# Performance work log

Measured on AMD Instinct MI355X. Metric: run time of the kernel, lower is better.

## Reference

```python
import jax, jax.numpy as jnp
import numpy as np

B, S, HID = 2, 2048, 1024
H, D = 16, 64  # head_dim = HID // H
MAXPOS = 2048


def setup_inputs() -> dict:
    key = jax.random.key(0)
    ks = jax.random.split(key, 9)
    s = 0.02
    return {
        "hidden_states": jax.random.normal(ks[0], (B, S, HID), jnp.float32),
        "attention_mask": jnp.zeros((B, 1, 1, S), jnp.float32),
        "Wq": jax.random.normal(ks[1], (HID, HID), jnp.float32) * s,
        "bq": jnp.zeros((HID,), jnp.float32),
        "Wk": jax.random.normal(ks[2], (HID, HID), jnp.float32) * s,
        "bk": jnp.zeros((HID,), jnp.float32),
        "Wv": jax.random.normal(ks[3], (HID, HID), jnp.float32) * s,
        "bv": jnp.zeros((HID,), jnp.float32),
        "dist_emb": jax.random.normal(ks[4], (2 * MAXPOS - 1, D), jnp.float32) * s,
    }


def reference(hidden_states, attention_mask, Wq, bq, Wk, bk, Wv, bv, dist_emb):
    b, s, _ = hidden_states.shape

    def heads(x):  # [B,S,HID] -> [B,H,S,D]
        return x.reshape(b, s, H, D).transpose(0, 2, 1, 3)

    q = heads(hidden_states @ Wq.T + bq)
    k = heads(hidden_states @ Wk.T + bk)
    v = heads(hidden_states @ Wv.T + bv)

    # raw scores [B,H,L,R]
    scores = jnp.einsum("bhld,bhrd->bhlr", q, k)

    # relative_key_query position bias
    pos_l = jnp.arange(s)[:, None]
    pos_r = jnp.arange(s)[None, :]
    distance = pos_l - pos_r + (MAXPOS - 1)  # [L,R]
    pos_emb = dist_emb[distance]  # [L,R,D]
    rel_q = jnp.einsum("bhld,lrd->bhlr", q, pos_emb)
    rel_k = jnp.einsum("bhrd,lrd->bhlr", k, pos_emb)
    scores = scores + rel_q + rel_k

    scores = scores / jnp.sqrt(jnp.asarray(D, scores.dtype))
    scores = scores + attention_mask  # additive mask broadcast [B,1,1,R]

    probs = jax.nn.softmax(scores, axis=-1)  # dropout p=0 -> identity
    ctx = jnp.einsum("bhlr,bhrd->bhld", probs, v)  # [B,H,L,D]
    ctx = ctx.transpose(0, 2, 1, 3).reshape(b, s, H * D)
    return ctx
```

## Files before the change

kernel.cpp:

```cpp
#include <hip/hip_runtime.h>

typedef __bf16 bf16_t;
typedef __bf16 bf16x8 __attribute__((ext_vector_type(8)));
typedef __bf16 bf16x4v __attribute__((ext_vector_type(4)));
typedef float floatx4 __attribute__((ext_vector_type(4)));

#define MFMA16(a, b, c) __builtin_amdgcn_mfma_f32_16x16x32_bf16((a), (b), (c), 0, 0, 0)

constexpr int S_ = 2048;
constexpr int HID_ = 1024;
constexpr int HH = 16;
constexpr int DD = 64;
constexpr float ALPHA = 0.125f * 1.44269504f;
constexpr float LOG2E = 1.44269504f;

__device__ __forceinline__ void async_copy16(const bf16_t* g, bf16_t* l) {
  __builtin_amdgcn_global_load_lds((const __attribute__((address_space(1))) unsigned int*)g,
                                   (__attribute__((address_space(3))) unsigned int*)l, 16, 0, 0);
}

__global__ __launch_bounds__(256) void cvt_all_kernel(
    const float* __restrict__ h, const float* __restrict__ wq, const float* __restrict__ wk,
    const float* __restrict__ wv, const float* __restrict__ de, bf16_t* __restrict__ hb,
    bf16_t* __restrict__ wb, bf16_t* __restrict__ eb) {
  int v = blockIdx.x * 256 + threadIdx.x;
  if (v >= 1900528) return;
  const float* src;
  bf16_t* dst;
  int off;
  if (v < 1048576) {
    src = h; dst = hb; off = v;
  } else if (v < 1310720) {
    src = wq; dst = wb; off = v - 1048576;
  } else if (v < 1572864) {
    src = wk; dst = wb + 1048576; off = v - 1310720;
  } else if (v < 1835008) {
    src = wv; dst = wb + 2097152; off = v - 1572864;
  } else {
    src = de; dst = eb; off = v - 1835008;
  }
  float4 f = *(const float4*)(src + (size_t)off * 4);
  bf16x4v p = {(bf16_t)f.x, (bf16_t)f.y, (bf16_t)f.z, (bf16_t)f.w};
  *(bf16x4v*)(dst + (size_t)off * 4) = p;
}

__global__ __launch_bounds__(256) void cvt_e_kernel(const float* __restrict__ src,
                                                    bf16_t* __restrict__ dst, int n) {
  int i = blockIdx.x * 256 + threadIdx.x;
  if (i < n) dst[i] = (bf16_t)src[i];
}

__global__ __launch_bounds__(256) void qkv_gemm3_kernel(
    const bf16_t* __restrict__ hb, const bf16_t* __restrict__ wb,
    const float* __restrict__ bq, const float* __restrict__ bk, const float* __restrict__ bv,
    bf16_t* __restrict__ qb, bf16_t* __restrict__ kb, bf16_t* __restrict__ vb) {
  __shared__ alignas(16) bf16_t As[128 * 64];
  __shared__ alignas(16) bf16_t Bs[128 * 64];
  const int tid = threadIdx.x;
  const int lane = tid & 63, wid = tid >> 6;
  const int l15 = lane & 15, quad = lane >> 4;
  const int m0 = blockIdx.x * 128, n0 = blockIdx.y * 128;
  const int wm = (wid >> 1) * 64, wn = (wid & 1) * 64;
  floatx4 acc[4][4] = {};
  const int srow = wid * 8 + (lane >> 3);
  const int scol = (lane & 7) * 8;
  const bf16_t* aptr = hb + (size_t)(m0 + srow) * HID_ + scol;
  const bf16_t* bptr = wb + (size_t)(n0 + srow) * HID_ + scol;
  bf16_t* As_w = As + (size_t)(wid * 8) * 64;
  bf16_t* Bs_w = Bs + (size_t)(wid * 8) * 64;

  for (int k0 = 0; k0 < HID_; k0 += 64) {
    __syncthreads();
#pragma unroll
    for (int p = 0; p < 4; ++p) {
      async_copy16(aptr + k0 + (size_t)p * 32 * HID_, As_w + p * 32 * 64);
      async_copy16(bptr + k0 + (size_t)p * 32 * HID_, Bs_w + p * 32 * 64);
    }
    __syncthreads();
    bf16x8 af[4][2], bfv[4][2];
#pragma unroll
    for (int t = 0; t < 4; ++t)
#pragma unroll
      for (int kh = 0; kh < 2; ++kh) {
        af[t][kh] = *(const bf16x8*)&As[(wm + t * 16 + l15) * 64 + kh * 32 + quad * 8];
        bfv[t][kh] = *(const bf16x8*)&Bs[(wn + t * 16 + l15) * 64 + kh * 32 + quad * 8];
      }
#pragma unroll
    for (int mt = 0; mt < 4; ++mt)
#pragma unroll
      for (int nt = 0; nt < 4; ++nt) {
        acc[mt][nt] = MFMA16(af[mt][0], bfv[nt][0], acc[mt][nt]);
        acc[mt][nt] = MFMA16(af[mt][1], bfv[nt][1], acc[mt][nt]);
      }
  }

  const int z = n0 >> 10;
  const float* bias = (z == 0) ? bq : (z == 1) ? bk : bv;
  bf16_t* out = (z == 0) ? qb : (z == 1) ? kb : vb;
  const float scl = (z == 0) ? ALPHA : 1.0f;
#pragma unroll
  for (int nt = 0; nt < 4; ++nt) {
    int oo = (n0 & 1023) + wn + nt * 16 + l15;
    float bvs = bias[oo];
    int h = oo >> 6, d = oo & 63;
#pragma unroll
    for (int mt = 0; mt < 4; ++mt) {
      int sb = m0 + wm + mt * 16 + quad * 4;
      int b = sb >> 11, s = sb & 2047;
      if (z != 2) {
        bf16_t* dst = out + (((size_t)(b * HH + h) * S_ + s) * DD + d);
#pragma unroll
        for (int i = 0; i < 4; ++i) dst[(size_t)i * DD] = (bf16_t)((acc[mt][nt][i] + bvs) * scl);
      } else {
        bf16_t* dst = out + (((size_t)(b * HH + h) * DD + d) * S_ + s);
        bf16x4v pk = {(bf16_t)(acc[mt][nt][0] + bvs), (bf16_t)(acc[mt][nt][1] + bvs),
                      (bf16_t)(acc[mt][nt][2] + bvs), (bf16_t)(acc[mt][nt][3] + bvs)};
        *(bf16x4v*)dst = pk;
      }
    }
  }
}

__global__ __launch_bounds__(256) void qkv_gemm_kernel(
    const float* __restrict__ X, const float* __restrict__ W,
    const float* __restrict__ bias, bf16_t* __restrict__ out, int transposed, float scl) {
  __shared__ alignas(16) bf16_t As[128][40];
  __shared__ alignas(16) bf16_t Bs[128][40];
  const int tid = threadIdx.x;
  const int lane = tid & 63, wid = tid >> 6;
  const int l15 = lane & 15, quad = lane >> 4;
  const int m0 = blockIdx.x * 128, n0 = blockIdx.y * 128;
  const int wm = (wid >> 1) * 64, wn = (wid & 1) * 64;
  floatx4 acc[4][4] = {};
  const int srow = tid >> 1, scol = (tid & 1) * 16;
  const float* aptr = X + (size_t)(m0 + srow) * HID_ + scol;
  const float* bptr = W + (size_t)(n0 + srow) * HID_ + scol;

  for (int k0 = 0; k0 < HID_; k0 += 32) {
    __syncthreads();
    {
      const float4* a4 = (const float4*)(aptr + k0);
      float4 f0 = a4[0], f1 = a4[1], f2 = a4[2], f3 = a4[3];
      bf16x4v p0 = {(bf16_t)f0.x, (bf16_t)f0.y, (bf16_t)f0.z, (bf16_t)f0.w};
      bf16x4v p1 = {(bf16_t)f1.x, (bf16_t)f1.y, (bf16_t)f1.z, (bf16_t)f1.w};
      bf16x4v p2 = {(bf16_t)f2.x, (bf16_t)f2.y, (bf16_t)f2.z, (bf16_t)f2.w};
      bf16x4v p3 = {(bf16_t)f3.x, (bf16_t)f3.y, (bf16_t)f3.z, (bf16_t)f3.w};
      *(bf16x4v*)&As[srow][scol + 0] = p0;
      *(bf16x4v*)&As[srow][scol + 4] = p1;
      *(bf16x4v*)&As[srow][scol + 8] = p2;
      *(bf16x4v*)&As[srow][scol + 12] = p3;
      const float4* b4 = (const float4*)(bptr + k0);
      float4 g0 = b4[0], g1 = b4[1], g2 = b4[2], g3 = b4[3];
      bf16x4v q0 = {(bf16_t)g0.x, (bf16_t)g0.y, (bf16_t)g0.z, (bf16_t)g0.w};
      bf16x4v q1 = {(bf16_t)g1.x, (bf16_t)g1.y, (bf16_t)g1.z, (bf16_t)g1.w};
      bf16x4v q2 = {(bf16_t)g2.x, (bf16_t)g2.y, (bf16_t)g2.z, (bf16_t)g2.w};
      bf16x4v q3 = {(bf16_t)g3.x, (bf16_t)g3.y, (bf16_t)g3.z, (bf16_t)g3.w};
      *(bf16x4v*)&Bs[srow][scol + 0] = q0;
      *(bf16x4v*)&Bs[srow][scol + 4] = q1;
      *(bf16x4v*)&Bs[srow][scol + 8] = q2;
      *(bf16x4v*)&Bs[srow][scol + 12] = q3;
    }
    __syncthreads();
    bf16x8 af[4], bfv[4];
#pragma unroll
    for (int t = 0; t < 4; ++t) af[t] = *(const bf16x8*)&As[wm + t * 16 + l15][quad * 8];
#pragma unroll
    for (int t = 0; t < 4; ++t) bfv[t] = *(const bf16x8*)&Bs[wn + t * 16 + l15][quad * 8];
#pragma unroll
    for (int mt = 0; mt < 4; ++mt)
#pragma unroll
      for (int nt = 0; nt < 4; ++nt)
        acc[mt][nt] = MFMA16(af[mt], bfv[nt], acc[mt][nt]);
  }

#pragma unroll
  for (int nt = 0; nt < 4; ++nt) {
    int o = n0 + wn + nt * 16 + l15;
    float bv = bias[o];
    int h = o >> 6, d = o & 63;
#pragma unroll
    for (int mt = 0; mt < 4; ++mt) {
      int sb = m0 + wm + mt * 16 + quad * 4;
      int b = sb >> 11, s = sb & 2047;
      if (!transposed) {
        bf16_t* dst = out + (((size_t)(b * HH + h) * S_ + s) * DD + d);
#pragma unroll
        for (int i = 0; i < 4; ++i) dst[(size_t)i * DD] = (bf16_t)((acc[mt][nt][i] + bv) * scl);
      } else {
        bf16_t* dst = out + (((size_t)(b * HH + h) * DD + d) * S_ + s);
        bf16x4v pk = {(bf16_t)(acc[mt][nt][0] + bv), (bf16_t)(acc[mt][nt][1] + bv),
                      (bf16_t)(acc[mt][nt][2] + bv), (bf16_t)(acc[mt][nt][3] + bv)};
        *(bf16x4v*)dst = pk;
      }
    }
  }
}

__global__ __launch_bounds__(256, 3) void attn8_kernel(
    const bf16_t* __restrict__ Q, const bf16_t* __restrict__ K,
    const bf16_t* __restrict__ Vt, const bf16_t* __restrict__ E,
    const float* __restrict__ mask, float* __restrict__ out) {
  __shared__ alignas(16) bf16_t Er[128 * 64];
  __shared__ alignas(16) bf16_t Vs[64 * 64];
  __shared__ alignas(16) bf16_t PX[65 * 64];
  __shared__ alignas(16) bf16_t X1t[64][134];
  __shared__ float lsumS[4][64];

  const int tid = threadIdx.x;
  const int lane = tid & 63, wid = tid >> 6;
  const int l15 = lane & 15, quad = lane >> 4;
  const int bh = blockIdx.x & 31, lblk = blockIdx.x >> 5;
  const int l0 = lblk * 64;
  const bf16_t* Qb = Q + (size_t)bh * S_ * DD;
  const bf16_t* Kb = K + (size_t)bh * S_ * DD;
  const bf16_t* Vb = Vt + (size_t)bh * DD * S_;
  const float* maskb = mask + (size_t)(bh >> 4) * S_;

  bf16x8 qB[4][2];
#pragma unroll
  for (int ct = 0; ct < 4; ++ct) {
    const bf16_t* qp = Qb + (size_t)(l0 + ct * 16 + l15) * DD + quad * 8;
    qB[ct][0] = *(const bf16x8*)qp;
    qB[ct][1] = *(const bf16x8*)(qp + 32);
  }

  {
    int rr = tid >> 2, c0 = (tid & 3) * 2;
    int grow = l0 + 2048 + rr;
    if (grow > 4094) grow = 4094;
    const bf16_t* ep = E + (size_t)grow * DD + c0 * 8;
    bf16x8 e0 = *(const bf16x8*)ep;
    bf16x8 e1 = *(const bf16x8*)(ep + 8);
    int slot = (l0 + 2048 + rr) & 127, sw = rr & 7;
    *(bf16x8*)&Er[slot * 64 + (((c0 + 0) ^ sw) << 3)] = e0;
    *(bf16x8*)&Er[slot * 64 + (((c0 + 1) ^ sw) << 3)] = e1;
  }
  __syncthreads();

#pragma unroll
  for (int wt = 0; wt < 4; ++wt) {
    int sr = (l0 + 2048 + wt * 16 + l15) & 127;
    int sw = l15 & 7;
    bf16x8 e0 = *(const bf16x8*)&Er[sr * 64 + ((quad ^ sw) << 3)];
    bf16x8 e1 = *(const bf16x8*)&Er[sr * 64 + (((4 + quad) ^ sw) << 3)];
    floatx4 t1 = {};
    t1 = MFMA16(qB[wid][0], e0, t1);
    t1 = MFMA16(qB[wid][1], e1, t1);
    const int wl = wt * 16 + l15;
#pragma unroll
    for (int i = 0; i < 4; ++i) {
      int ll = wid * 16 + quad * 4 + i;
      int r = ll - wl - 1;
      int col = (r >= 0) ? r : (128 + i);
      X1t[ll][col] = (bf16_t)t1[i];
    }
  }

  floatx4 Oacc[4] = {};
  float lsum[4] = {0.f, 0.f, 0.f, 0.f};

  for (int r0 = 0; r0 < S_; r0 += 64) {
    const int A = l0 - r0 + 1984;
    {
      int rr = tid >> 2, c0 = (tid & 3) * 2;
      const bf16_t* ep = E + (size_t)(A + rr) * DD + c0 * 8;
      bf16x8 e0 = *(const bf16x8*)ep;
      bf16x8 e1 = *(const bf16x8*)(ep + 8);
      int slot = (A + rr) & 127, sw = rr & 7;
      *(bf16x8*)&Er[slot * 64 + (((c0 + 0) ^ sw) << 3)] = e0;
      *(bf16x8*)&Er[slot * 64 + (((c0 + 1) ^ sw) << 3)] = e1;
    }
    const bf16_t* kp = Kb + (size_t)(r0 + wid * 16 + l15) * DD + quad * 8;
    bf16x8 kf0 = *(const bf16x8*)kp;
    bf16x8 kf1 = *(const bf16x8*)(kp + 32);
    float4 m4 = *(const float4*)(maskb + r0 + wid * 16 + quad * 4);
    float mlg[4] = {m4.x * LOG2E, m4.y * LOG2E, m4.z * LOG2E, m4.w * LOG2E};
    __syncthreads();

#pragma unroll
    for (int wt = 0; wt < 8; ++wt) {
      const bool needT1 = (wt < 4);
      const bool needT2 = (wt + wid >= 3) && (wt + wid <= 7);
      if (!(needT1 || needT2)) continue;
      int sr = (A + wt * 16 + l15) & 127;
      int sw = l15 & 7;
      bf16x8 e0 = *(const bf16x8*)&Er[sr * 64 + ((quad ^ sw) << 3)];
      bf16x8 e1 = *(const bf16x8*)&Er[sr * 64 + (((4 + quad) ^ sw) << 3)];
      const int wl = wt * 16 + l15;
      if (needT2) {
        floatx4 t2 = {};
        t2 = MFMA16(kf0, e0, t2);
        t2 = MFMA16(kf1, e1, t2);
#pragma unroll
        for (int i = 0; i < 4; ++i) {
          int rl = wid * 16 + quad * 4 + i;
          int ll = rl + wl - 63;
          int row = ((unsigned)ll < 64u) ? ll : 64;
          int col = (((rl >> 3) ^ (row & 7)) << 3) + (rl & 7);
          PX[row * 64 + col] = (bf16_t)(t2[i] * ALPHA + mlg[i]);
        }
      }
      if (needT1) {
        floatx4 t1 = {};
        t1 = MFMA16(qB[wid][0], e0, t1);
        t1 = MFMA16(qB[wid][1], e1, t1);
#pragma unroll
        for (int i = 0; i < 4; ++i) {
          int ll = wid * 16 + quad * 4 + i;
          int rc = (r0 + 63 + ll - wl) & 127;
          X1t[ll][rc] = (bf16_t)t1[i];
        }
      }
    }
    {
      int row = tid >> 2, c0 = (tid & 3) * 2;
      const bf16_t* vp = Vb + (size_t)row * S_ + r0 + c0 * 8;
      bf16x8 v0 = *(const bf16x8*)vp;
      bf16x8 v1 = *(const bf16x8*)(vp + 8);
      int h7 = row & 7;
      *(bf16x8*)&Vs[row * 64 + (((c0 + 0) ^ h7) << 3)] = v0;
      *(bf16x8*)&Vs[row * 64 + (((c0 + 1) ^ h7) << 3)] = v1;
    }
    __syncthreads();

    const int xc = (r0 + wid * 16 + quad * 4) & 127;
    const int pc = wid * 2 + (quad >> 1);
#pragma unroll
    for (int ct = 0; ct < 4; ++ct) {
      floatx4 s = {};
      s = MFMA16(kf0, qB[ct][0], s);
      s = MFMA16(kf1, qB[ct][1], s);
      bf16x4v x1 = *(const bf16x4v*)&X1t[ct * 16 + l15][xc];
      const int row = ct * 16 + l15;
      bf16_t* px = &PX[row * 64 + (((pc ^ (row & 7)) << 3) + ((quad & 1) << 2))];
      bf16x4v x2 = *(const bf16x4v*)px;
      bf16x4v pk;
#pragma unroll
      for (int i = 0; i < 4; ++i) {
        float sv = s[i] + (float)x1[i] + (float)x2[i];
        float p = __builtin_amdgcn_exp2f(sv);
        lsum[ct] += p;
        pk[i] = (bf16_t)p;
      }
      *(bf16x4v*)px = pk;
    }
    __syncthreads();

    {
      const int prow = wid * 16 + l15;
      const int ph = prow & 7;
      bf16x8 pf0 = *(const bf16x8*)&PX[prow * 64 + ((quad ^ ph) << 3)];
      bf16x8 pf1 = *(const bf16x8*)&PX[prow * 64 + (((4 + quad) ^ ph) << 3)];
#pragma unroll
      for (int dt = 0; dt < 4; ++dt) {
        int vrow = dt * 16 + l15;
        int vh = vrow & 7;
        bf16x8 v0 = *(const bf16x8*)&Vs[vrow * 64 + ((quad ^ vh) << 3)];
        bf16x8 v1 = *(const bf16x8*)&Vs[vrow * 64 + (((4 + quad) ^ vh) << 3)];
        Oacc[dt] = MFMA16(v0, pf0, Oacc[dt]);
        Oacc[dt] = MFMA16(v1, pf1, Oacc[dt]);
      }
    }
  }

#pragma unroll
  for (int ct = 0; ct < 4; ++ct) {
    lsum[ct] += __shfl_xor(lsum[ct], 16);
    lsum[ct] += __shfl_xor(lsum[ct], 32);
  }
  __syncthreads();
  if (quad == 0) {
#pragma unroll
    for (int ct = 0; ct < 4; ++ct) lsumS[wid][ct * 16 + l15] = lsum[ct];
  }
  __syncthreads();
  const int lidx = wid * 16 + l15;
  float tot = lsumS[0][lidx] + lsumS[1][lidx] + lsumS[2][lidx] + lsumS[3][lidx];
  float inv = 1.f / tot;
  const int b = bh >> 4, h = bh & 15;
  float* dst = out + (size_t)(b * S_ + l0 + lidx) * HID_ + h * DD + quad * 4;
#pragma unroll
  for (int dt = 0; dt < 4; ++dt) {
    float4 o = {Oacc[dt][0] * inv, Oacc[dt][1] * inv, Oacc[dt][2] * inv, Oacc[dt][3] * inv};
    *(float4*)(dst + dt * 16) = o;
  }
}

extern "C" void kernel_launch(void* const* d_in, const int* in_sizes, int n_in,
                              void* d_out, int out_size, void* d_ws, size_t ws_size,
                              hipStream_t stream) {
  const float* hidden = (const float*)d_in[0];
  const float* amask = (const float*)d_in[1];
  const float* Wq = (const float*)d_in[2];
  const float* bq = (const float*)d_in[3];
  const float* Wk = (const float*)d_in[4];
  const float* bk = (const float*)d_in[5];
  const float* Wv = (const float*)d_in[6];
  const float* bv = (const float*)d_in[7];
  const float* de = (const float*)d_in[8];
  float* outp = (float*)d_out;
  char* ws = (char*)d_ws;
  const size_t MB = 1024 * 1024;
  bf16_t* qb = (bf16_t*)(ws);
  bf16_t* kb = (bf16_t*)(ws + 8 * MB);
  bf16_t* vb = (bf16_t*)(ws + 16 * MB);
  bf16_t* eb = (bf16_t*)(ws + 24 * MB);
  bf16_t* hb = (bf16_t*)(ws + 25 * MB);
  bf16_t* wb = (bf16_t*)(ws + 33 * MB);

  if (ws_size >= 39 * MB) {
    cvt_all_kernel<<<dim3(7424), 256, 0, stream>>>(hidden, Wq, Wk, Wv, de, hb, wb, eb);
    qkv_gemm3_kernel<<<dim3(32, 24), 256, 0, stream>>>(hb, wb, bq, bk, bv, qb, kb, vb);
  } else {
    cvt_e_kernel<<<dim3(1024), 256, 0, stream>>>(de, eb, 4095 * 64);
    dim3 g(32, 8);
    qkv_gemm_kernel<<<g, 256, 0, stream>>>(hidden, Wq, bq, qb, 0, ALPHA);
    qkv_gemm_kernel<<<g, 256, 0, stream>>>(hidden, Wk, bk, kb, 0, 1.0f);
    qkv_gemm_kernel<<<g, 256, 0, stream>>>(hidden, Wv, bv, vb, 1, 1.0f);
  }
  attn8_kernel<<<dim3(1024), 256, 0, stream>>>(qb, kb, vb, eb, amask, outp);
}
```

Before: 303.8 us.

## Shrink attention LDS footprint, cache E fragments in registers, remap QKV GEMM grid

The attention kernel packs its shared buffers into one aliased 40 KB region, replacing the padded X1t with a rotated 128-column layout, so four blocks can fit per CU instead of three. E tiles are now stored in a 64-row LDS window, and the previous window's fragments are kept in registers (eC), which removes redundant LDS reads for the key-position bias term. Out-of-range scratch writes become predicated. The QKV GEMM switches to a 1D grid that groups M tiles per XCD to improve L2 reuse, at the cost of more register pressure and more complex indexing in attention.

```diff
diff --git a/kernel.cpp b/kernel.cpp
--- a/kernel.cpp
+++ b/kernel.cpp
@@ -50,7 +50,7 @@
   if (i < n) dst[i] = (bf16_t)src[i];
 }
 
-__global__ __launch_bounds__(256) void qkv_gemm3_kernel(
+__global__ __launch_bounds__(256) void qkv_gemm4_kernel(
     const bf16_t* __restrict__ hb, const bf16_t* __restrict__ wb,
     const float* __restrict__ bq, const float* __restrict__ bk, const float* __restrict__ bv,
     bf16_t* __restrict__ qb, bf16_t* __restrict__ kb, bf16_t* __restrict__ vb) {
@@ -59,13 +59,16 @@
   const int tid = threadIdx.x;
   const int lane = tid & 63, wid = tid >> 6;
   const int l15 = lane & 15, quad = lane >> 4;
-  const int m0 = blockIdx.x * 128, n0 = blockIdx.y * 128;
+  const int bidx = blockIdx.x;
+  const int xcd = bidx & 7, idx = bidx >> 3;
+  const int m0 = (xcd * 4 + (idx & 3)) * 128;
+  const int nAbs = (idx >> 2) * 128;
   const int wm = (wid >> 1) * 64, wn = (wid & 1) * 64;
   floatx4 acc[4][4] = {};
   const int srow = wid * 8 + (lane >> 3);
   const int scol = (lane & 7) * 8;
   const bf16_t* aptr = hb + (size_t)(m0 + srow) * HID_ + scol;
-  const bf16_t* bptr = wb + (size_t)(n0 + srow) * HID_ + scol;
+  const bf16_t* bptr = wb + (size_t)(nAbs + srow) * HID_ + scol;
   bf16_t* As_w = As + (size_t)(wid * 8) * 64;
   bf16_t* Bs_w = Bs + (size_t)(wid * 8) * 64;
 
@@ -94,13 +97,13 @@
       }
   }
 
-  const int z = n0 >> 10;
+  const int z = nAbs >> 10;
   const float* bias = (z == 0) ? bq : (z == 1) ? bk : bv;
   bf16_t* out = (z == 0) ? qb : (z == 1) ? kb : vb;
   const float scl = (z == 0) ? ALPHA : 1.0f;
 #pragma unroll
   for (int nt = 0; nt < 4; ++nt) {
-    int oo = (n0 & 1023) + wn + nt * 16 + l15;
+    int oo = (nAbs & 1023) + wn + nt * 16 + l15;
     float bvs = bias[oo];
     int h = oo >> 6, d = oo & 63;
 #pragma unroll
@@ -196,15 +199,16 @@
   }
 }
 
-__global__ __launch_bounds__(256, 3) void attn8_kernel(
+__global__ __launch_bounds__(256, 4) void attn9_kernel(
     const bf16_t* __restrict__ Q, const bf16_t* __restrict__ K,
     const bf16_t* __restrict__ Vt, const bf16_t* __restrict__ E,
     const float* __restrict__ mask, float* __restrict__ out) {
-  __shared__ alignas(16) bf16_t Er[128 * 64];
-  __shared__ alignas(16) bf16_t Vs[64 * 64];
-  __shared__ alignas(16) bf16_t PX[65 * 64];
-  __shared__ alignas(16) bf16_t X1t[64][134];
-  __shared__ float lsumS[4][64];
+  __shared__ alignas(16) char smem[40960];
+  bf16_t* X1t = (bf16_t*)smem;
+  bf16_t* Er = (bf16_t*)(smem + 16384);
+  bf16_t* Vs = (bf16_t*)(smem + 24576);
+  bf16_t* PX = (bf16_t*)(smem + 32768);
+  float* lsumS = (float*)(smem + 16384);
 
   const int tid = threadIdx.x;
   const int lane = tid & 63, wid = tid >> 6;
@@ -224,6 +228,8 @@
     qB[ct][1] = *(const bf16x8*)(qp + 32);
   }
 
+  bf16x8 eC[4][2];
+
   {
     int rr = tid >> 2, c0 = (tid & 3) * 2;
     int grow = l0 + 2048 + rr;
@@ -231,18 +237,17 @@
     const bf16_t* ep = E + (size_t)grow * DD + c0 * 8;
     bf16x8 e0 = *(const bf16x8*)ep;
     bf16x8 e1 = *(const bf16x8*)(ep + 8);
-    int slot = (l0 + 2048 + rr) & 127, sw = rr & 7;
-    *(bf16x8*)&Er[slot * 64 + (((c0 + 0) ^ sw) << 3)] = e0;
-    *(bf16x8*)&Er[slot * 64 + (((c0 + 1) ^ sw) << 3)] = e1;
+    int sw = rr & 7;
+    *(bf16x8*)&Er[rr * 64 + (((c0 + 0) ^ sw) << 3)] = e0;
+    *(bf16x8*)&Er[rr * 64 + (((c0 + 1) ^ sw) << 3)] = e1;
   }
   __syncthreads();
-
 #pragma unroll
   for (int wt = 0; wt < 4; ++wt) {
-    int sr = (l0 + 2048 + wt * 16 + l15) & 127;
+    int slot = wt * 16 + l15;
     int sw = l15 & 7;
-    bf16x8 e0 = *(const bf16x8*)&Er[sr * 64 + ((quad ^ sw) << 3)];
-    bf16x8 e1 = *(const bf16x8*)&Er[sr * 64 + (((4 + quad) ^ sw) << 3)];
+    bf16x8 e0 = *(const bf16x8*)&Er[slot * 64 + ((quad ^ sw) << 3)];
+    bf16x8 e1 = *(const bf16x8*)&Er[slot * 64 + (((4 + quad) ^ sw) << 3)];
     floatx4 t1 = {};
     t1 = MFMA16(qB[wid][0], e0, t1);
     t1 = MFMA16(qB[wid][1], e1, t1);
@@ -251,10 +256,12 @@
     for (int i = 0; i < 4; ++i) {
       int ll = wid * 16 + quad * 4 + i;
       int r = ll - wl - 1;
-      int col = (r >= 0) ? r : (128 + i);
-      X1t[ll][col] = (bf16_t)t1[i];
-    }
-  }
+      if (r >= 0) X1t[ll * 128 + ((((r >> 2) + ll) & 31) << 2) + (r & 3)] = (bf16_t)t1[i];
+    }
+    eC[wt][0] = e0;
+    eC[wt][1] = e1;
+  }
+  __syncthreads();
 
   floatx4 Oacc[4] = {};
   float lsum[4] = {0.f, 0.f, 0.f, 0.f};
@@ -266,9 +273,9 @@
       const bf16_t* ep = E + (size_t)(A + rr) * DD + c0 * 8;
       bf16x8 e0 = *(const bf16x8*)ep;
       bf16x8 e1 = *(const bf16x8*)(ep + 8);
-      int slot = (A + rr) & 127, sw = rr & 7;
-      *(bf16x8*)&Er[slot * 64 + (((c0 + 0) ^ sw) << 3)] = e0;
-      *(bf16x8*)&Er[slot * 64 + (((c0 + 1) ^ sw) << 3)] = e1;
+      int sw = rr & 7;
+      *(bf16x8*)&Er[rr * 64 + (((c0 + 0) ^ sw) << 3)] = e0;
+      *(bf16x8*)&Er[rr * 64 + (((c0 + 1) ^ sw) << 3)] = e1;
     }
     const bf16_t* kp = Kb + (size_t)(r0 + wid * 16 + l15) * DD + quad * 8;
     bf16x8 kf0 = *(const bf16x8*)kp;
@@ -278,16 +285,29 @@
     __syncthreads();
 
 #pragma unroll
-    for (int wt = 0; wt < 8; ++wt) {
-      const bool needT1 = (wt < 4);
-      const bool needT2 = (wt + wid >= 3) && (wt + wid <= 7);
-      if (!(needT1 || needT2)) continue;
-      int sr = (A + wt * 16 + l15) & 127;
+    for (int wt = 4; wt < 8; ++wt) {
+      if (wt <= 7 - wid) {
+        floatx4 t2 = {};
+        t2 = MFMA16(kf0, eC[wt - 4][0], t2);
+        t2 = MFMA16(kf1, eC[wt - 4][1], t2);
+        const int wl = wt * 16 + l15;
+#pragma unroll
+        for (int i = 0; i < 4; ++i) {
+          int rl = wid * 16 + quad * 4 + i;
+          int ll = rl + wl - 63;
+          if ((unsigned)ll < 64u)
+            PX[ll * 64 + ((((rl >> 3) ^ (ll & 7)) << 3) + (rl & 7))] = (bf16_t)(t2[i] * ALPHA + mlg[i]);
+        }
+      }
+    }
+#pragma unroll
+    for (int wt = 0; wt < 4; ++wt) {
+      int slot = wt * 16 + l15;
       int sw = l15 & 7;
-      bf16x8 e0 = *(const bf16x8*)&Er[sr * 64 + ((quad ^ sw) << 3)];
-      bf16x8 e1 = *(const bf16x8*)&Er[sr * 64 + (((4 + quad) ^ sw) << 3)];
+      bf16x8 e0 = *(const bf16x8*)&Er[slot * 64 + ((quad ^ sw) << 3)];
+      bf16x8 e1 = *(const bf16x8*)&Er[slot * 64 + (((4 + quad) ^ sw) << 3)];
       const int wl = wt * 16 + l15;
-      if (needT2) {
+      if (wt >= 3 - wid) {
         floatx4 t2 = {};
         t2 = MFMA16(kf0, e0, t2);
         t2 = MFMA16(kf1, e1, t2);
@@ -295,12 +315,11 @@
         for (int i = 0; i < 4; ++i) {
           int rl = wid * 16 + quad * 4 + i;
           int ll = rl + wl - 63;
-          int row = ((unsigned)ll < 64u) ? ll : 64;
-          int col = (((rl >> 3) ^ (row & 7)) << 3) + (rl & 7);
-          PX[row * 64 + col] = (bf16_t)(t2[i] * ALPHA + mlg[i]);
+          if ((unsigned)ll < 64u)
+            PX[ll * 64 + ((((rl >> 3) ^ (ll & 7)) << 3) + (rl & 7))] = (bf16_t)(t2[i] * ALPHA + mlg[i]);
         }
       }
-      if (needT1) {
+      {
         floatx4 t1 = {};
         t1 = MFMA16(qB[wid][0], e0, t1);
         t1 = MFMA16(qB[wid][1], e1, t1);
@@ -308,9 +327,11 @@
         for (int i = 0; i < 4; ++i) {
           int ll = wid * 16 + quad * 4 + i;
           int rc = (r0 + 63 + ll - wl) & 127;
-          X1t[ll][rc] = (bf16_t)t1[i];
+          X1t[ll * 128 + ((((rc >> 2) + ll) & 31) << 2) + (rc & 3)] = (bf16_t)t1[i];
         }
       }
+      eC[wt][0] = e0;
+      eC[wt][1] = e1;
     }
     {
       int row = tid >> 2, c0 = (tid & 3) * 2;
@@ -324,14 +345,15 @@
     __syncthreads();
 
     const int xc = (r0 + wid * 16 + quad * 4) & 127;
+    const int xc4 = xc >> 2;
     const int pc = wid * 2 + (quad >> 1);
 #pragma unroll
     for (int ct = 0; ct < 4; ++ct) {
       floatx4 s = {};
       s = MFMA16(kf0, qB[ct][0], s);
       s = MFMA16(kf1, qB[ct][1], s);
-      bf16x4v x1 = *(const bf16x4v*)&X1t[ct * 16 + l15][xc];
       const int row = ct * 16 + l15;
+      bf16x4v x1 = *(const bf16x4v*)&X1t[row * 128 + (((xc4 + row) & 31) << 2)];
       bf16_t* px = &PX[row * 64 + (((pc ^ (row & 7)) << 3) + ((quad & 1) << 2))];
       bf16x4v x2 = *(const bf16x4v*)px;
       bf16x4v pk;
@@ -371,11 +393,11 @@
   __syncthreads();
   if (quad == 0) {
 #pragma unroll
-    for (int ct = 0; ct < 4; ++ct) lsumS[wid][ct * 16 + l15] = lsum[ct];
+    for (int ct = 0; ct < 4; ++ct) lsumS[wid * 64 + ct * 16 + l15] = lsum[ct];
   }
   __syncthreads();
   const int lidx = wid * 16 + l15;
-  float tot = lsumS[0][lidx] + lsumS[1][lidx] + lsumS[2][lidx] + lsumS[3][lidx];
+  float tot = lsumS[lidx] + lsumS[64 + lidx] + lsumS[128 + lidx] + lsumS[192 + lidx];
   float inv = 1.f / tot;
   const int b = bh >> 4, h = bh & 15;
   float* dst = out + (size_t)(b * S_ + l0 + lidx) * HID_ + h * DD + quad * 4;
@@ -410,7 +432,7 @@
 
   if (ws_size >= 39 * MB) {
     cvt_all_kernel<<<dim3(7424), 256, 0, stream>>>(hidden, Wq, Wk, Wv, de, hb, wb, eb);
-    qkv_gemm3_kernel<<<dim3(32, 24), 256, 0, stream>>>(hb, wb, bq, bk, bv, qb, kb, vb);
+    qkv_gemm4_kernel<<<dim3(768), 256, 0, stream>>>(hb, wb, bq, bk, bv, qb, kb, vb);
   } else {
     cvt_e_kernel<<<dim3(1024), 256, 0, stream>>>(de, eb, 4095 * 64);
     dim3 g(32, 8);
@@ -418,5 +440,5 @@
     qkv_gemm_kernel<<<g, 256, 0, stream>>>(hidden, Wk, bk, kb, 0, 1.0f);
     qkv_gemm_kernel<<<g, 256, 0, stream>>>(hidden, Wv, bv, vb, 1, 1.0f);
   }
-  attn8_kernel<<<dim3(1024), 256, 0, stream>>>(qb, kb, vb, eb, amask, outp);
-}
+  attn9_kernel<<<dim3(1024), 256, 0, stream>>>(qb, kb, vb, eb, amask, outp);
+}
```

Measured after the change: 643.0 us. 112% more time.
